# Optimization experiments

Measured on AMD Instinct MI355X. Metric: run time of the kernel, lower is better.

The kernel has to match this reference:

```python
import jax, jax.numpy as jnp
import numpy as np

B, C, H, W = 8, 64, 128, 128
CH = 3 * C      # MS_CAM channels = channels*3 = 192
IC = CH // 2    # inter_channels with r=2 = 96
EPS = 1e-5


def _conv1x1(x, w, b):
    # x: [B, Cin, H, W], w: [Cout, Cin], b: [Cout]
    return jnp.einsum('bchw,oc->bohw', x, w) + b[:, None, None]


def _bn(x, g, beta, mean, var):
    # eval-mode BatchNorm2d over channel axis 1
    scale = g / jnp.sqrt(var + EPS)
    return (x - mean[:, None, None]) * scale[:, None, None] + beta[:, None, None]


def setup_inputs() -> dict:
    key = jax.random.key(0)
    ks = jax.random.split(key, 24)
    f = lambda i, s, sc=1.0: jax.random.normal(ks[i], s, jnp.float32) * sc
    d = {
        'x1': f(0, (B, C, H, W)),
        'x2': f(1, (B, C, H, W)),
        'x3': f(2, (B, C, H, W)),
    }
    def make_path(prefix, off):
        d[prefix + 'w1'] = f(off + 0, (IC, CH), 0.05)
        d[prefix + 'b1'] = f(off + 1, (IC,), 0.05)
        d[prefix + 'g1'] = jnp.ones((IC,), jnp.float32)
        d[prefix + 'be1'] = jnp.zeros((IC,), jnp.float32)
        d[prefix + 'm1'] = f(off + 2, (IC,), 0.05)
        d[prefix + 'v1'] = jax.random.uniform(ks[off + 3], (IC,), jnp.float32) + 0.5
        d[prefix + 'w2'] = f(off + 4, (CH, IC), 0.05)
        d[prefix + 'b2'] = f(off + 5, (CH,), 0.05)
        d[prefix + 'g2'] = jnp.ones((CH,), jnp.float32)
        d[prefix + 'be2'] = jnp.zeros((CH,), jnp.float32)
        d[prefix + 'm2'] = f(off + 6, (CH,), 0.05)
        d[prefix + 'v2'] = jax.random.uniform(ks[off + 7], (CH,), jnp.float32) + 0.5
    make_path('l', 3)   # local_att params
    make_path('g', 12)  # global_att params
    return d


def _att_branch(x, w1, b1, g1, be1, m1, v1, w2, b2, g2, be2, m2, v2):
    h = jax.nn.relu(_bn(_conv1x1(x, w1, b1), g1, be1, m1, v1))
    return _bn(_conv1x1(h, w2, b2), g2, be2, m2, v2)


def reference(x1, x2, x3,
              lw1, lb1, lg1, lbe1, lm1, lv1, lw2, lb2, lg2, lbe2, lm2, lv2,
              gw1, gb1, gg1, gbe1, gm1, gv1, gw2, gb2, gg2, gbe2, gm2, gv2):
    # MS_CAM: concat, local (per-pixel) + global (GAP) channel attention
    x = jnp.concatenate([x1, x2, x3], axis=1)                      # [B, 3C, H, W]
    xl = _att_branch(x, lw1, lb1, lg1, lbe1, lm1, lv1, lw2, lb2, lg2, lbe2, lm2, lv2)
    xg = _att_branch(jnp.mean(x, axis=(2, 3), keepdims=True),      # [B, 3C, 1, 1]
                     gw1, gb1, gg1, gbe1, gm1, gv1, gw2, gb2, gg2, gbe2, gm2, gv2)
    wei = jax.nn.sigmoid(xl + xg)                                  # [B, 3C, H, W]

    # FUB edge/node matrices + per-pixel 1x3 @ 3x1 bmm collapse to a fused
    # softmax-over-3 weighted sum (identical flatten order on both sides).
    w = jnp.stack([wei[:, 0:C], wei[:, C:2 * C], wei[:, 2 * C:]], axis=0)  # [3,B,C,H,W]
    w = jax.nn.softmax(w, axis=0)
    xs = jnp.stack([x1, x2, x3], axis=0)                           # [3,B,C,H,W]
    return jnp.sum(w * xs, axis=0)                                 # [B,C,H,W]
```

## Files before the change

kernel.cpp:

```cpp
#include <hip/hip_runtime.h>

#define HWPIX 16384
#define XSTR 200
#define HSTR 104

typedef float f32x4 __attribute__((ext_vector_type(4)));
typedef short s16x8 __attribute__((ext_vector_type(8)));

static __device__ __forceinline__ unsigned short f2bf(float f) {
    unsigned int u = __builtin_bit_cast(unsigned int, f);
    u += 0x7fffu + ((u >> 16) & 1u);
    return (unsigned short)(u >> 16);
}
static __device__ __forceinline__ unsigned int pack2(float lo, float hi) {
    return (unsigned int)f2bf(lo) | ((unsigned int)f2bf(hi) << 16);
}
static __device__ __forceinline__ float bf2f(unsigned short u) {
    unsigned int x = ((unsigned int)u) << 16;
    return __builtin_bit_cast(float, x);
}


__global__ __launch_bounds__(256) void prep_kernel(
    const float* __restrict__ x1, const float* __restrict__ x2, const float* __restrict__ x3,
    const float* __restrict__ lw1, const float* __restrict__ lb1,
    const float* __restrict__ lg1, const float* __restrict__ lbe1,
    const float* __restrict__ lm1, const float* __restrict__ lv1,
    const float* __restrict__ lw2, const float* __restrict__ lb2,
    const float* __restrict__ lg2, const float* __restrict__ lbe2,
    const float* __restrict__ lm2, const float* __restrict__ lv2,
    float* __restrict__ wsf, unsigned short* __restrict__ w1f, unsigned short* __restrict__ w2f)
{
    const int bid = blockIdx.x, t = threadIdx.x;
    if (bid < 1536) {
        int b = bid / 192, c = bid % 192;
        int g = c >> 6, cc = c & 63;
        const float* base = (g == 0 ? x1 : (g == 1 ? x2 : x3)) + ((size_t)(b * 64 + cc)) * HWPIX;
        float s = 0.f;
        #pragma unroll
        for (int it = 0; it < 16; ++it) {
            f32x4 v = *(const f32x4*)(base + it * 1024 + t * 4);
            s += v[0] + v[1] + v[2] + v[3];
        }
        for (int off = 32; off > 0; off >>= 1) s += __shfl_down(s, off, 64);
        __shared__ float part[4];
        if ((t & 63) == 0) part[t >> 6] = s;
        __syncthreads();
        if (t == 0) wsf[bid] = (part[0] + part[1] + part[2] + part[3]) * (1.f / (float)HWPIX);
    } else if (bid == 1536) {
        if (t < 96) {
            float s = lg1[t] * __frsqrt_rn(lv1[t] + 1e-5f);
            wsf[3072 + t] = s;
            wsf[3168 + t] = (lb1[t] - lm1[t]) * s + lbe1[t];
        }
    } else if (bid == 1537) {
        if (t < 192) {
            float s = lg2[t] * __frsqrt_rn(lv2[t] + 1e-5f);
            wsf[3264 + t] = s;
            wsf[3456 + t] = (lb2[t] - lm2[t]) * s + lbe2[t];
        }
    } else if (bid < 1547) {
        int slot = (bid - 1538) * 256 + t;
        int f = slot >> 6, l = slot & 63;
        int kb = f / 6, nb = f % 6;
        int row = nb * 16 + (l & 15), col0 = kb * 32 + ((l >> 4) << 3);
        const float* src = lw1 + row * 192 + col0;
        f32x4 a = *(const f32x4*)src, b4 = *(const f32x4*)(src + 4);
        unsigned int* dst = (unsigned int*)(w1f + f * 512 + l * 8);
        dst[0] = pack2(a[0], a[1]); dst[1] = pack2(a[2], a[3]);
        dst[2] = pack2(b4[0], b4[1]); dst[3] = pack2(b4[2], b4[3]);
    } else {
        int slot = (bid - 1547) * 256 + t;
        int f = slot >> 6, l = slot & 63;
        int kb = f / 12, nb = f % 12;
        int row = nb * 16 + (l & 15), col0 = kb * 32 + ((l >> 4) << 3);
        const float* src = lw2 + row * 96 + col0;
        f32x4 a = *(const f32x4*)src, b4 = *(const f32x4*)(src + 4);
        unsigned int* dst = (unsigned int*)(w2f + f * 512 + l * 8);
        dst[0] = pack2(a[0], a[1]); dst[1] = pack2(a[2], a[3]);
        dst[2] = pack2(b4[0], b4[1]); dst[3] = pack2(b4[2], b4[3]);
    }
}

__global__ __launch_bounds__(256) void gpath_kernel(
    const float* __restrict__ gw1, const float* __restrict__ gb1,
    const float* __restrict__ gg1, const float* __restrict__ gbe1,
    const float* __restrict__ gm1, const float* __restrict__ gv1,
    const float* __restrict__ gw2, const float* __restrict__ gb2,
    const float* __restrict__ gg2, const float* __restrict__ gbe2,
    const float* __restrict__ gm2, const float* __restrict__ gv2,
    float* __restrict__ wsf)
{
    __shared__ float xbar[192], hbuf[96];
    const int b = blockIdx.x, t = threadIdx.x;
    if (t < 192) xbar[t] = wsf[b * 192 + t];
    __syncthreads();
    if (t < 96) {
        float acc = 0.f;
        for (int c = 0; c < 192; ++c) acc += gw1[t * 192 + c] * xbar[c];
        float s = gg1[t] * __frsqrt_rn(gv1[t] + 1e-5f);
        float tt = (gb1[t] - gm1[t]) * s + gbe1[t];
        hbuf[t] = fmaxf(acc * s + tt, 0.f);
    }
    __syncthreads();
    if (t < 192) {
        float acc = 0.f;
        for (int j = 0; j < 96; ++j) acc += gw2[t * 96 + j] * hbuf[j];
        float s = gg2[t] * __frsqrt_rn(gv2[t] + 1e-5f);
        float tt = (gb2[t] - gm2[t]) * s + gbe2[t];
        wsf[1536 + b * 192 + t] = acc * s + tt;
    }
}

__global__ __launch_bounds__(256, 2) void main_kernel(
    const float* __restrict__ x1, const float* __restrict__ x2, const float* __restrict__ x3,
    const float* __restrict__ wsf,
    const unsigned short* __restrict__ w1f, const unsigned short* __restrict__ w2f,
    float* __restrict__ out)
{
    __shared__ __align__(16) unsigned short lx[64 * XSTR];
    __shared__ __align__(16) unsigned short lw[18 * 512];
    __shared__ __align__(16) unsigned short lh[64 * HSTR];
    __shared__ float lpar[768];

    const int t = threadIdx.x;
    const int b = blockIdx.x >> 8;
    const int pix0 = (blockIdx.x & 255) << 6;

    if (t < 96)  { lpar[t] = wsf[3072 + t]; lpar[96 + t] = wsf[3168 + t]; }
    if (t < 192) {
        lpar[192 + t] = wsf[3264 + t];
        lpar[384 + t] = wsf[3456 + t];
        lpar[576 + t] = wsf[1536 + b * 192 + t];
    }
    {
        const int pq = t >> 4;
        const int cb = t & 15;
        unsigned int* lx32 = (unsigned int*)lx;
        #pragma unroll
        for (int i = 0; i < 6; ++i) {
            int cp = i * 16 + cb;
            int c0 = cp * 2;
            int g = c0 >> 6, cc0 = c0 & 63;
            const float* pl = (g == 0 ? x1 : (g == 1 ? x2 : x3))
                + ((size_t)(b * 64 + cc0)) * HWPIX + pix0 + pq * 4;
            f32x4 va = *(const f32x4*)pl;
            f32x4 vb = *(const f32x4*)(pl + HWPIX);
            #pragma unroll
            for (int j = 0; j < 4; ++j)
                lx32[(pq * 4 + j) * 100 + cp] = pack2(va[j], vb[j]);
        }
    }
    #pragma unroll
    for (int i = 0; i < 5; ++i) {
        int slot = i * 256 + t;
        if (slot < 1152) ((uint4*)lw)[slot] = ((const uint4*)w1f)[slot];
    }
    __syncthreads();

    const int lane = t & 63;
    const int wv = t >> 6;
    const int col = lane & 15;
    const int q = lane >> 4;
    const int pixw = wv * 16;

    f32x4 acc1[6];
    #pragma unroll
    for (int nb = 0; nb < 6; ++nb) acc1[nb] = (f32x4){0.f, 0.f, 0.f, 0.f};

    #pragma unroll
    for (int half = 0; half < 2; ++half) {
        if (half == 1) {
            __syncthreads();
            #pragma unroll
            for (int i = 0; i < 5; ++i) {
                int slot = i * 256 + t;
                if (slot < 1152) ((uint4*)lw)[slot] = ((const uint4*)w1f)[1152 + slot];
            }
            __syncthreads();
        }
        #pragma unroll
        for (int kbl = 0; kbl < 3; ++kbl) {
            int kb = half * 3 + kbl;
            s16x8 a = *(const s16x8*)&lx[(pixw + col) * XSTR + kb * 32 + q * 8];
            #pragma unroll
            for (int nb = 0; nb < 6; ++nb) {
                s16x8 bfr = *(const s16x8*)&lw[(kbl * 6 + nb) * 512 + lane * 8];
                acc1[nb] = __builtin_amdgcn_mfma_f32_16x16x32_bf16(a, bfr, acc1[nb], 0, 0, 0);
            }
        }
    }
    #pragma unroll
    for (int nb = 0; nb < 6; ++nb) {
        int j = nb * 16 + col;
        float sj = lpar[j], tj = lpar[96 + j];
        #pragma unroll
        for (int r = 0; r < 4; ++r) {
            int pix = pixw + q * 4 + r;
            lh[pix * HSTR + j] = f2bf(fmaxf(acc1[nb][r] * sj + tj, 0.f));
        }
    }

    f32x4 acc2[12];
    #pragma unroll
    for (int nb = 0; nb < 12; ++nb) acc2[nb] = (f32x4){0.f, 0.f, 0.f, 0.f};

    #pragma unroll
    for (int kb = 0; kb < 3; ++kb) {
        __syncthreads();
        #pragma unroll
        for (int i = 0; i < 3; ++i) {
            int slot = i * 256 + t;
            ((uint4*)lw)[slot] = ((const uint4*)w2f)[kb * 768 + slot];
        }
        __syncthreads();
        s16x8 a = *(const s16x8*)&lh[(pixw + col) * HSTR + kb * 32 + q * 8];
        #pragma unroll
        for (int nb = 0; nb < 12; ++nb) {
            s16x8 bfr = *(const s16x8*)&lw[nb * 512 + lane * 8];
            acc2[nb] = __builtin_amdgcn_mfma_f32_16x16x32_bf16(a, bfr, acc2[nb], 0, 0, 0);
        }
    }

    #pragma unroll
    for (int nb = 0; nb < 4; ++nb) {
        int cc = nb * 16 + col;
        float s0 = lpar[192 + cc],        t0 = lpar[384 + cc],        g0 = lpar[576 + cc];
        float s1v = lpar[192 + 64 + cc],  t1v = lpar[384 + 64 + cc],  g1 = lpar[576 + 64 + cc];
        float s2v = lpar[192 + 128 + cc], t2v = lpar[384 + 128 + cc], g2 = lpar[576 + 128 + cc];
        size_t po = ((size_t)(b * 64 + cc)) * HWPIX + pix0 + pixw + q * 4;
        f32x4 xa = *(const f32x4*)(x1 + po);
        f32x4 xb = *(const f32x4*)(x2 + po);
        f32x4 xc = *(const f32x4*)(x3 + po);
        f32x4 res;
        #pragma unroll
        for (int r = 0; r < 4; ++r) {
            float v0 = acc2[nb][r] * s0 + t0 + g0;
            float v1 = acc2[nb + 4][r] * s1v + t1v + g1;
            float v2 = acc2[nb + 8][r] * s2v + t2v + g2;
            float w0 = 1.f / (1.f + __expf(-v0));
            float w1 = 1.f / (1.f + __expf(-v1));
            float w2 = 1.f / (1.f + __expf(-v2));
            float mx = fmaxf(w0, fmaxf(w1, w2));
            float e0 = __expf(w0 - mx), e1 = __expf(w1 - mx), e2 = __expf(w2 - mx);
            res[r] = (e0 * xa[r] + e1 * xb[r] + e2 * xc[r]) / (e0 + e1 + e2);
        }
        *(f32x4*)(out + po) = res;
    }
}

extern "C" void kernel_launch(void* const* d_in, const int* in_sizes, int n_in,
                              void* d_out, int out_size, void* d_ws, size_t ws_size,
                              hipStream_t stream) {
    (void)in_sizes; (void)n_in; (void)out_size; (void)ws_size;
    const float* x1  = (const float*)d_in[0];
    const float* x2  = (const float*)d_in[1];
    const float* x3  = (const float*)d_in[2];
    const float* lw1 = (const float*)d_in[3];
    const float* lb1 = (const float*)d_in[4];
    const float* lg1 = (const float*)d_in[5];
    const float* lbe1= (const float*)d_in[6];
    const float* lm1 = (const float*)d_in[7];
    const float* lv1 = (const float*)d_in[8];
    const float* lw2 = (const float*)d_in[9];
    const float* lb2 = (const float*)d_in[10];
    const float* lg2 = (const float*)d_in[11];
    const float* lbe2= (const float*)d_in[12];
    const float* lm2 = (const float*)d_in[13];
    const float* lv2 = (const float*)d_in[14];
    const float* gw1 = (const float*)d_in[15];
    const float* gb1 = (const float*)d_in[16];
    const float* gg1 = (const float*)d_in[17];
    const float* gbe1= (const float*)d_in[18];
    const float* gm1 = (const float*)d_in[19];
    const float* gv1 = (const float*)d_in[20];
    const float* gw2 = (const float*)d_in[21];
    const float* gb2 = (const float*)d_in[22];
    const float* gg2 = (const float*)d_in[23];
    const float* gbe2= (const float*)d_in[24];
    const float* gm2 = (const float*)d_in[25];
    const float* gv2 = (const float*)d_in[26];

    float* wsf = (float*)d_ws;
    unsigned short* w1f = (unsigned short*)((char*)d_ws + 16384);
    unsigned short* w2f = w1f + 18432;

    prep_kernel<<<1556, 256, 0, stream>>>(x1, x2, x3,
        lw1, lb1, lg1, lbe1, lm1, lv1, lw2, lb2, lg2, lbe2, lm2, lv2,
        wsf, w1f, w2f);
    gpath_kernel<<<8, 256, 0, stream>>>(
        gw1, gb1, gg1, gbe1, gm1, gv1, gw2, gb2, gg2, gbe2, gm2, gv2, wsf);
    main_kernel<<<2048, 256, 0, stream>>>(x1, x2, x3, wsf, w1f, w2f, (float*)d_out);
}
```

Before: 236.1 us.

## Double-buffer weight chunks via global_load_lds and alias hidden buffer onto input tile

Weight tiles for both 1x1-conv GEMMs now stream into two ping-pong LDS buffers with direct global-to-LDS loads. Each next chunk is issued before the MFMAs on the current chunk, so weight fetches overlap compute instead of sitting between barriers. The hidden activation buffer now reuses each wave's own rows of the input tile, and occupancy is raised to 3 blocks per CU to match the smaller LDS footprint. The risks are the ordering of the direct-to-LDS loads, which now depends on barriers with no explicit vmcnt wait, and added register pressure at the higher occupancy.

Result: faster. 229.9 us (-2.6%).

```diff
diff --git a/kernel.cpp b/kernel.cpp
--- a/kernel.cpp
+++ b/kernel.cpp
@@ -15,9 +15,23 @@
 static __device__ __forceinline__ unsigned int pack2(float lo, float hi) {
     return (unsigned int)f2bf(lo) | ((unsigned int)f2bf(hi) << 16);
 }
-static __device__ __forceinline__ float bf2f(unsigned short u) {
-    unsigned int x = ((unsigned int)u) << 16;
-    return __builtin_bit_cast(float, x);
+
+static __device__ __forceinline__ void gll16(const void* g, void* l) {
+    __builtin_amdgcn_global_load_lds(
+        (const __attribute__((address_space(1))) unsigned int*)g,
+        (__attribute__((address_space(3))) unsigned int*)l,
+        16, 0, 0);
+}
+
+static __device__ __forceinline__ void stage_chunk(const unsigned short* gsrc,
+                                                   unsigned short* lbuf,
+                                                   int wv, int lane) {
+    #pragma unroll
+    for (int i = 0; i < 3; ++i) {
+        int rr = wv * 3 + i;
+        gll16((const char*)gsrc + rr * 1024 + lane * 16,
+              (char*)lbuf + rr * 1024);
+    }
 }
 
 
@@ -112,20 +126,23 @@
     }
 }
 
-__global__ __launch_bounds__(256, 2) void main_kernel(
+__global__ __launch_bounds__(256, 3) void main_kernel(
     const float* __restrict__ x1, const float* __restrict__ x2, const float* __restrict__ x3,
     const float* __restrict__ wsf,
     const unsigned short* __restrict__ w1f, const unsigned short* __restrict__ w2f,
     float* __restrict__ out)
 {
     __shared__ __align__(16) unsigned short lx[64 * XSTR];
-    __shared__ __align__(16) unsigned short lw[18 * 512];
-    __shared__ __align__(16) unsigned short lh[64 * HSTR];
+    __shared__ __align__(16) unsigned short lw[2][12 * 512];
     __shared__ float lpar[768];
 
     const int t = threadIdx.x;
     const int b = blockIdx.x >> 8;
     const int pix0 = (blockIdx.x & 255) << 6;
+    const int lane = t & 63;
+    const int wv = t >> 6;
+
+    stage_chunk(w1f, lw[0], wv, lane);
 
     if (t < 96)  { lpar[t] = wsf[3072 + t]; lpar[96 + t] = wsf[3168 + t]; }
     if (t < 192) {
@@ -151,76 +168,69 @@
                 lx32[(pq * 4 + j) * 100 + cp] = pack2(va[j], vb[j]);
         }
     }
-    #pragma unroll
-    for (int i = 0; i < 5; ++i) {
-        int slot = i * 256 + t;
-        if (slot < 1152) ((uint4*)lw)[slot] = ((const uint4*)w1f)[slot];
-    }
-    __syncthreads();
-
-    const int lane = t & 63;
-    const int wv = t >> 6;
+    __syncthreads();
+
     const int col = lane & 15;
     const int q = lane >> 4;
     const int pixw = wv * 16;
+    unsigned short* lhp = &lx[pixw * XSTR];
+
+    stage_chunk(w1f + 12 * 512, lw[1], wv, lane);
 
     f32x4 acc1[6];
     #pragma unroll
     for (int nb = 0; nb < 6; ++nb) acc1[nb] = (f32x4){0.f, 0.f, 0.f, 0.f};
 
-    #pragma unroll
-    for (int half = 0; half < 2; ++half) {
-        if (half == 1) {
-            __syncthreads();
-            #pragma unroll
-            for (int i = 0; i < 5; ++i) {
-                int slot = i * 256 + t;
-                if (slot < 1152) ((uint4*)lw)[slot] = ((const uint4*)w1f)[1152 + slot];
-            }
-            __syncthreads();
-        }
-        #pragma unroll
-        for (int kbl = 0; kbl < 3; ++kbl) {
-            int kb = half * 3 + kbl;
-            s16x8 a = *(const s16x8*)&lx[(pixw + col) * XSTR + kb * 32 + q * 8];
-            #pragma unroll
-            for (int nb = 0; nb < 6; ++nb) {
-                s16x8 bfr = *(const s16x8*)&lw[(kbl * 6 + nb) * 512 + lane * 8];
-                acc1[nb] = __builtin_amdgcn_mfma_f32_16x16x32_bf16(a, bfr, acc1[nb], 0, 0, 0);
-            }
-        }
-    }
+#define P1_STEP(BUF, KB0)                                                              \
+    _Pragma("unroll")                                                                  \
+    for (int kbl = 0; kbl < 2; ++kbl) {                                                \
+        s16x8 a = *(const s16x8*)&lx[(pixw + col) * XSTR + (KB0 + kbl) * 32 + q * 8];  \
+        _Pragma("unroll")                                                              \
+        for (int nb = 0; nb < 6; ++nb) {                                               \
+            s16x8 bfr = *(const s16x8*)&lw[BUF][(kbl * 6 + nb) * 512 + lane * 8];      \
+            acc1[nb] = __builtin_amdgcn_mfma_f32_16x16x32_bf16(a, bfr, acc1[nb], 0, 0, 0); \
+        }                                                                              \
+    }
+
+    P1_STEP(0, 0)
+    __syncthreads();
+    stage_chunk(w1f + 24 * 512, lw[0], wv, lane);
+    P1_STEP(1, 2)
+    __syncthreads();
+    stage_chunk(w2f, lw[1], wv, lane);
+    P1_STEP(0, 4)
+
     #pragma unroll
     for (int nb = 0; nb < 6; ++nb) {
         int j = nb * 16 + col;
         float sj = lpar[j], tj = lpar[96 + j];
         #pragma unroll
-        for (int r = 0; r < 4; ++r) {
-            int pix = pixw + q * 4 + r;
-            lh[pix * HSTR + j] = f2bf(fmaxf(acc1[nb][r] * sj + tj, 0.f));
-        }
-    }
+        for (int r = 0; r < 4; ++r)
+            lhp[(q * 4 + r) * HSTR + j] = f2bf(fmaxf(acc1[nb][r] * sj + tj, 0.f));
+    }
+    __syncthreads();
+    stage_chunk(w2f + 12 * 512, lw[0], wv, lane);
 
     f32x4 acc2[12];
     #pragma unroll
     for (int nb = 0; nb < 12; ++nb) acc2[nb] = (f32x4){0.f, 0.f, 0.f, 0.f};
 
-    #pragma unroll
-    for (int kb = 0; kb < 3; ++kb) {
-        __syncthreads();
-        #pragma unroll
-        for (int i = 0; i < 3; ++i) {
-            int slot = i * 256 + t;
-            ((uint4*)lw)[slot] = ((const uint4*)w2f)[kb * 768 + slot];
-        }
-        __syncthreads();
-        s16x8 a = *(const s16x8*)&lh[(pixw + col) * HSTR + kb * 32 + q * 8];
-        #pragma unroll
-        for (int nb = 0; nb < 12; ++nb) {
-            s16x8 bfr = *(const s16x8*)&lw[nb * 512 + lane * 8];
-            acc2[nb] = __builtin_amdgcn_mfma_f32_16x16x32_bf16(a, bfr, acc2[nb], 0, 0, 0);
-        }
-    }
+#define P2_STEP(BUF, KB)                                                               \
+    {                                                                                  \
+        s16x8 a = *(const s16x8*)&lhp[col * HSTR + (KB) * 32 + q * 8];                 \
+        _Pragma("unroll")                                                              \
+        for (int nb = 0; nb < 12; ++nb) {                                              \
+            s16x8 bfr = *(const s16x8*)&lw[BUF][nb * 512 + lane * 8];                  \
+            acc2[nb] = __builtin_amdgcn_mfma_f32_16x16x32_bf16(a, bfr, acc2[nb], 0, 0, 0); \
+        }                                                                              \
+    }
+
+    P2_STEP(1, 0)
+    __syncthreads();
+    stage_chunk(w2f + 24 * 512, lw[1], wv, lane);
+    P2_STEP(0, 1)
+    __syncthreads();
+    P2_STEP(1, 2)
 
     #pragma unroll
     for (int nb = 0; nb < 4; ++nb) {
```

## Read weights directly from global, reuse lx for hidden tile, raise occupancy

Applied to the files above, without the earlier changes.

Drops the shared-memory weight staging buffers and their block-wide barriers, so MFMA B-fragments are loaded straight from global/L2. The hidden activations now reuse each wave's own rows of the input tile instead of a separate buffer. Shrinking LDS lets launch bounds request 4 blocks per CU. The epilogue folds BN scale, shift and the global branch into exp2 constants, uses hardware rcp/exp2, drops the softmax max subtraction (safe because sigmoid outputs lie in [0,1]), and converts to bf16 with v_cvt_pk_bf16_f32. Global weight reads may add latency in exchange for fewer barriers and more waves.

Result: faster. 228.0 us (-3.4%).

```diff
diff --git a/kernel.cpp b/kernel.cpp
--- a/kernel.cpp
+++ b/kernel.cpp
@@ -3,6 +3,7 @@
 #define HWPIX 16384
 #define XSTR 200
 #define HSTR 104
+#define L2E 1.4426950408889634f
 
 typedef float f32x4 __attribute__((ext_vector_type(4)));
 typedef short s16x8 __attribute__((ext_vector_type(8)));
@@ -15,9 +16,10 @@
 static __device__ __forceinline__ unsigned int pack2(float lo, float hi) {
     return (unsigned int)f2bf(lo) | ((unsigned int)f2bf(hi) << 16);
 }
-static __device__ __forceinline__ float bf2f(unsigned short u) {
-    unsigned int x = ((unsigned int)u) << 16;
-    return __builtin_bit_cast(float, x);
+static __device__ __forceinline__ unsigned int cvtpk(float lo, float hi) {
+    unsigned int r;
+    asm("v_cvt_pk_bf16_f32 %0, %1, %2" : "=v"(r) : "v"(lo), "v"(hi));
+    return r;
 }
 
 
@@ -112,26 +114,26 @@
     }
 }
 
-__global__ __launch_bounds__(256, 2) void main_kernel(
+__global__ __launch_bounds__(256, 4) void main_kernel(
     const float* __restrict__ x1, const float* __restrict__ x2, const float* __restrict__ x3,
     const float* __restrict__ wsf,
     const unsigned short* __restrict__ w1f, const unsigned short* __restrict__ w2f,
     float* __restrict__ out)
 {
     __shared__ __align__(16) unsigned short lx[64 * XSTR];
-    __shared__ __align__(16) unsigned short lw[18 * 512];
-    __shared__ __align__(16) unsigned short lh[64 * HSTR];
-    __shared__ float lpar[768];
+    __shared__ float lpar[576];
 
     const int t = threadIdx.x;
     const int b = blockIdx.x >> 8;
     const int pix0 = (blockIdx.x & 255) << 6;
+    const int lane = t & 63;
+    const int wv = t >> 6;
 
     if (t < 96)  { lpar[t] = wsf[3072 + t]; lpar[96 + t] = wsf[3168 + t]; }
     if (t < 192) {
-        lpar[192 + t] = wsf[3264 + t];
-        lpar[384 + t] = wsf[3456 + t];
-        lpar[576 + t] = wsf[1536 + b * 192 + t];
+        float s2 = wsf[3264 + t], t2 = wsf[3456 + t], xg = wsf[1536 + b * 192 + t];
+        lpar[192 + t] = -L2E * s2;
+        lpar[384 + t] = -L2E * (t2 + xg);
     }
     {
         const int pq = t >> 4;
@@ -148,56 +150,44 @@
             f32x4 vb = *(const f32x4*)(pl + HWPIX);
             #pragma unroll
             for (int j = 0; j < 4; ++j)
-                lx32[(pq * 4 + j) * 100 + cp] = pack2(va[j], vb[j]);
-        }
-    }
-    #pragma unroll
-    for (int i = 0; i < 5; ++i) {
-        int slot = i * 256 + t;
-        if (slot < 1152) ((uint4*)lw)[slot] = ((const uint4*)w1f)[slot];
+                lx32[(pq * 4 + j) * 100 + cp] = cvtpk(va[j], vb[j]);
+        }
     }
     __syncthreads();
 
-    const int lane = t & 63;
-    const int wv = t >> 6;
     const int col = lane & 15;
     const int q = lane >> 4;
     const int pixw = wv * 16;
+    unsigned short* lhp = &lx[pixw * XSTR];
 
     f32x4 acc1[6];
     #pragma unroll
     for (int nb = 0; nb < 6; ++nb) acc1[nb] = (f32x4){0.f, 0.f, 0.f, 0.f};
 
     #pragma unroll
-    for (int half = 0; half < 2; ++half) {
-        if (half == 1) {
-            __syncthreads();
-            #pragma unroll
-            for (int i = 0; i < 5; ++i) {
-                int slot = i * 256 + t;
-                if (slot < 1152) ((uint4*)lw)[slot] = ((const uint4*)w1f)[1152 + slot];
-            }
-            __syncthreads();
-        }
-        #pragma unroll
-        for (int kbl = 0; kbl < 3; ++kbl) {
-            int kb = half * 3 + kbl;
-            s16x8 a = *(const s16x8*)&lx[(pixw + col) * XSTR + kb * 32 + q * 8];
-            #pragma unroll
-            for (int nb = 0; nb < 6; ++nb) {
-                s16x8 bfr = *(const s16x8*)&lw[(kbl * 6 + nb) * 512 + lane * 8];
-                acc1[nb] = __builtin_amdgcn_mfma_f32_16x16x32_bf16(a, bfr, acc1[nb], 0, 0, 0);
-            }
-        }
-    }
-    #pragma unroll
-    for (int nb = 0; nb < 6; ++nb) {
-        int j = nb * 16 + col;
-        float sj = lpar[j], tj = lpar[96 + j];
+    for (int kb = 0; kb < 6; ++kb) {
+        s16x8 a = *(const s16x8*)&lx[(pixw + col) * XSTR + kb * 32 + q * 8];
+        const unsigned short* wp = w1f + (kb * 6) * 512 + lane * 8;
+        #pragma unroll
+        for (int nb = 0; nb < 6; ++nb) {
+            s16x8 bfr = *(const s16x8*)(wp + nb * 512);
+            acc1[nb] = __builtin_amdgcn_mfma_f32_16x16x32_bf16(a, bfr, acc1[nb], 0, 0, 0);
+        }
+    }
+
+    #pragma unroll
+    for (int nbp = 0; nbp < 3; ++nbp) {
+        int j0 = (2 * nbp) * 16 + col, j1 = (2 * nbp + 1) * 16 + col;
+        float s0 = lpar[j0], t0 = lpar[96 + j0];
+        float s1v = lpar[j1], t1v = lpar[96 + j1];
         #pragma unroll
         for (int r = 0; r < 4; ++r) {
-            int pix = pixw + q * 4 + r;
-            lh[pix * HSTR + j] = f2bf(fmaxf(acc1[nb][r] * sj + tj, 0.f));
+            float h0 = fmaxf(acc1[2 * nbp][r] * s0 + t0, 0.f);
+            float h1 = fmaxf(acc1[2 * nbp + 1][r] * s1v + t1v, 0.f);
+            unsigned int w = cvtpk(h0, h1);
+            int rowo = (q * 4 + r) * HSTR;
+            lhp[rowo + j0] = (unsigned short)w;
+            lhp[rowo + j1] = (unsigned short)(w >> 16);
         }
     }
 
@@ -207,17 +197,11 @@
 
     #pragma unroll
     for (int kb = 0; kb < 3; ++kb) {
-        __syncthreads();
-        #pragma unroll
-        for (int i = 0; i < 3; ++i) {
-            int slot = i * 256 + t;
-            ((uint4*)lw)[slot] = ((const uint4*)w2f)[kb * 768 + slot];
-        }
-        __syncthreads();
-        s16x8 a = *(const s16x8*)&lh[(pixw + col) * HSTR + kb * 32 + q * 8];
+        s16x8 a = *(const s16x8*)&lhp[col * HSTR + kb * 32 + q * 8];
+        const unsigned short* wp = w2f + (kb * 12) * 512 + lane * 8;
         #pragma unroll
         for (int nb = 0; nb < 12; ++nb) {
-            s16x8 bfr = *(const s16x8*)&lw[nb * 512 + lane * 8];
+            s16x8 bfr = *(const s16x8*)(wp + nb * 512);
             acc2[nb] = __builtin_amdgcn_mfma_f32_16x16x32_bf16(a, bfr, acc2[nb], 0, 0, 0);
         }
     }
@@ -225,9 +209,9 @@
     #pragma unroll
     for (int nb = 0; nb < 4; ++nb) {
         int cc = nb * 16 + col;
-        float s0 = lpar[192 + cc],        t0 = lpar[384 + cc],        g0 = lpar[576 + cc];
-        float s1v = lpar[192 + 64 + cc],  t1v = lpar[384 + 64 + cc],  g1 = lpar[576 + 64 + cc];
-        float s2v = lpar[192 + 128 + cc], t2v = lpar[384 + 128 + cc], g2 = lpar[576 + 128 + cc];
+        float A0 = lpar[192 + cc],       B0 = lpar[384 + cc];
+        float A1 = lpar[192 + 64 + cc],  B1 = lpar[384 + 64 + cc];
+        float A2 = lpar[192 + 128 + cc], B2 = lpar[384 + 128 + cc];
         size_t po = ((size_t)(b * 64 + cc)) * HWPIX + pix0 + pixw + q * 4;
         f32x4 xa = *(const f32x4*)(x1 + po);
         f32x4 xb = *(const f32x4*)(x2 + po);
@@ -235,15 +219,14 @@
         f32x4 res;
         #pragma unroll
         for (int r = 0; r < 4; ++r) {
-            float v0 = acc2[nb][r] * s0 + t0 + g0;
-            float v1 = acc2[nb + 4][r] * s1v + t1v + g1;
-            float v2 = acc2[nb + 8][r] * s2v + t2v + g2;
-            float w0 = 1.f / (1.f + __expf(-v0));
-            float w1 = 1.f / (1.f + __expf(-v1));
-            float w2 = 1.f / (1.f + __expf(-v2));
-            float mx = fmaxf(w0, fmaxf(w1, w2));
-            float e0 = __expf(w0 - mx), e1 = __expf(w1 - mx), e2 = __expf(w2 - mx);
-            res[r] = (e0 * xa[r] + e1 * xb[r] + e2 * xc[r]) / (e0 + e1 + e2);
+            float w0 = __builtin_amdgcn_rcpf(1.f + __builtin_amdgcn_exp2f(acc2[nb][r]     * A0 + B0));
+            float w1 = __builtin_amdgcn_rcpf(1.f + __builtin_amdgcn_exp2f(acc2[nb + 4][r] * A1 + B1));
+            float w2 = __builtin_amdgcn_rcpf(1.f + __builtin_amdgcn_exp2f(acc2[nb + 8][r] * A2 + B2));
+            float e0 = __builtin_amdgcn_exp2f(w0 * L2E);
+            float e1 = __builtin_amdgcn_exp2f(w1 * L2E);
+            float e2 = __builtin_amdgcn_exp2f(w2 * L2E);
+            float inv = __builtin_amdgcn_rcpf(e0 + e1 + e2);
+            res[r] = (e0 * xa[r] + e1 * xb[r] + e2 * xc[r]) * inv;
         }
         *(f32x4*)(out + po) = res;
     }
```
